# Optimization experiments

Measured on AMD Instinct MI355X. Metric: run time of the kernel, lower is better.

## Reference

```python
import jax, jax.numpy as jnp
import numpy as np
import math

D_MODEL = 1024
N_HEADS = 16
D_K = D_MODEL // N_HEADS
B, S = 4, 2048
NEG_INF = -1e9


def setup_inputs() -> dict:
    key = jax.random.key(0)
    ks = jax.random.split(key, 12)
    scale = 1.0 / math.sqrt(D_MODEL)
    inp = {
        "q": jax.random.normal(ks[0], (B, S, D_MODEL), jnp.float32),
        "k": jax.random.normal(ks[1], (B, S, D_MODEL), jnp.float32),
        "v": jax.random.normal(ks[2], (B, S, D_MODEL), jnp.float32),
        "mask": jax.random.randint(ks[3], (1, 1, S, S), 0, 2, jnp.int32),
        "w_q": jax.random.normal(ks[4], (D_MODEL, D_MODEL), jnp.float32) * scale,
        "b_q": jnp.zeros((D_MODEL,), jnp.float32),
        "w_k": jax.random.normal(ks[5], (D_MODEL, D_MODEL), jnp.float32) * scale,
        "b_k": jnp.zeros((D_MODEL,), jnp.float32),
        "w_v": jax.random.normal(ks[6], (D_MODEL, D_MODEL), jnp.float32) * scale,
        "b_v": jnp.zeros((D_MODEL,), jnp.float32),
        "w_o": jax.random.normal(ks[7], (D_MODEL, D_MODEL), jnp.float32) * scale,
        "b_o": jnp.zeros((D_MODEL,), jnp.float32),
    }
    return inp


def reference(q, k, v, mask, w_q, b_q, w_k, b_k, w_v, b_v, w_o, b_o):
    # Linear projections (torch Linear: x @ W.T + b)
    query = q @ w_q.T + b_q
    key_p = k @ w_k.T + b_k
    value = v @ w_v.T + b_v
    # [B,S,D] -> [B,H,S,d_k]
    def split_heads(x):
        return x.reshape(B, S, N_HEADS, D_K).transpose(0, 2, 1, 3)
    qh, kh, vh = split_heads(query), split_heads(key_p), split_heads(value)
    # scores: [B,H,S,S]
    scores = jnp.einsum('bhqd,bhkd->bhqk', qh, kh) / math.sqrt(D_K)
    scores = jnp.where(mask == 0, NEG_INF, scores)
    probs = jax.nn.softmax(scores, axis=-1)
    # attention output: [B,H,S,d_k] -> [B,S,D]
    x = jnp.einsum('bhqk,bhkd->bhqd', probs, vh)
    x = x.transpose(0, 2, 1, 3).reshape(B, S, D_MODEL)
    return x @ w_o.T + b_o
```

## Files before the change

kernel.cpp:

```cpp
#include <hip/hip_runtime.h>


typedef __bf16  bf16x8 __attribute__((ext_vector_type(8)));
typedef float   f32x4  __attribute__((ext_vector_type(4)));
typedef float   f32x16 __attribute__((ext_vector_type(16)));
typedef float   fv4    __attribute__((ext_vector_type(4)));
typedef unsigned int uint;
typedef __attribute__((address_space(3))) char        as3c;
typedef __attribute__((address_space(1))) const char  as1c;

static __device__ __forceinline__ void gload16(const void* g, void* l) {
  __builtin_amdgcn_global_load_lds((as1c*)g, (as3c*)l, 16, 0, 0);
}
static __device__ __forceinline__ f32x4 mfma16(bf16x8 a, bf16x8 b, f32x4 c) {
  return __builtin_amdgcn_mfma_f32_16x16x32_bf16(a, b, c, 0, 0, 0);
}
static __device__ __forceinline__ f32x16 mfma32(bf16x8 a, bf16x8 b, f32x16 c) {
  return __builtin_amdgcn_mfma_f32_32x32x16_bf16(a, b, c, 0, 0, 0);
}
static __device__ __forceinline__ void st4bf(void* dst, float a, float b, float c, float d) {
  union { __bf16 h[4]; unsigned long long u; } x;
  x.h[0] = (__bf16)a; x.h[1] = (__bf16)b; x.h[2] = (__bf16)c; x.h[3] = (__bf16)d;
  *(unsigned long long*)dst = x.u;
}
static __device__ __forceinline__ uint pk2(float lo, float hi) {
  union { __bf16 h[2]; uint u; } x;
  x.h[0] = (__bf16)lo; x.h[1] = (__bf16)hi; return x.u;
}
static __device__ __forceinline__ f32x16 fzero16() {
  f32x16 z;
#pragma unroll
  for (int i = 0; i < 16; ++i) z[i] = 0.f;
  return z;
}

__global__ void cvt_w(const float* __restrict__ w0, const float* __restrict__ w1,
                      const float* __restrict__ w2, const float* __restrict__ w3,
                      __bf16* __restrict__ dst) {
  int i = (blockIdx.x * 256 + threadIdx.x) * 4;
  int seg = i >> 20, off = i & 1048575;
  const float* s = seg == 0 ? w0 : seg == 1 ? w1 : seg == 2 ? w2 : w3;
  fv4 v = *(const fv4*)(s + off);
  st4bf(dst + i, v[0], v[1], v[2], v[3]);
}

__global__ void pack_mask(const int* __restrict__ mask,
                          unsigned long long* __restrict__ out) {
  int wid = threadIdx.x >> 6, lane = threadIdx.x & 63;
  for (int w = blockIdx.x * 4 + wid; w < 2048 * 32; w += gridDim.x * 4) {
    int v = mask[(w >> 5) * 2048 + (w & 31) * 64 + lane];
    unsigned long long bits = __ballot(v != 0);
    if (lane == 0) out[w] = bits;
  }
}

template<int MODE>
__global__ __launch_bounds__(256, 2)
void gemm_bt(const void* __restrict__ Ap, const __bf16* __restrict__ Bw,
             const float* __restrict__ bias, void* __restrict__ Cp) {
  __shared__ __align__(16) char lds_a[8192];
  __shared__ __align__(16) char lds_b[8192];
  const int t = threadIdx.x;
  const int lane = t & 63, lr = lane & 15, lg = lane >> 4;
  const int wid = t >> 6, wr = wid >> 1, wc = wid & 1;
  const int rowStart = blockIdx.x * 128, colStart = blockIdx.y * 128;

  f32x4 acc[4][4];
#pragma unroll
  for (int m = 0; m < 4; ++m)
#pragma unroll
    for (int n = 0; n < 4; ++n) {
      acc[m][n][0] = 0.f; acc[m][n][1] = 0.f; acc[m][n][2] = 0.f; acc[m][n][3] = 0.f;
    }

  for (int kt = 0; kt < 1024; kt += 32) {
    __syncthreads();
    if constexpr (MODE < 3) {
      const float* A = (const float*)Ap;
#pragma unroll
      for (int rr = 0; rr < 4; ++rr) {
        int lin = rr * 1024 + t * 4;
        int row = lin >> 5, col = lin & 31;
        fv4 v = *(const fv4*)(A + (rowStart + row) * 1024 + kt + col);
        st4bf(lds_a + lin * 2, v[0], v[1], v[2], v[3]);
      }
    } else {
      const __bf16* A = (const __bf16*)Ap;
#pragma unroll
      for (int rr = 0; rr < 2; ++rr) {
        int lin = rr * 2048 + t * 8;
        int row = lin >> 5, col = lin & 31;
        gload16(A + (rowStart + row) * 1024 + kt + col, lds_a + lin * 2);
      }
    }
#pragma unroll
    for (int rr = 0; rr < 2; ++rr) {
      int lin = rr * 2048 + t * 8;
      int row = lin >> 5, col = lin & 31;
      gload16(Bw + (colStart + row) * 1024 + kt + col, lds_b + lin * 2);
    }
    __syncthreads();

    bf16x8 af[4], bfr[4];
#pragma unroll
    for (int m = 0; m < 4; ++m)
      af[m] = *(const bf16x8*)(lds_a + (wr * 64 + m * 16 + lr) * 64 + lg * 16);
#pragma unroll
    for (int n = 0; n < 4; ++n)
      bfr[n] = *(const bf16x8*)(lds_b + (wc * 64 + n * 16 + lr) * 64 + lg * 16);
#pragma unroll
    for (int m = 0; m < 4; ++m)
#pragma unroll
      for (int n = 0; n < 4; ++n)
        acc[m][n] = mfma16(af[m], bfr[n], acc[m][n]);
  }

#pragma unroll
  for (int n = 0; n < 4; ++n) {
    int col = colStart + wc * 64 + n * 16 + lr;
    float bv = bias[col];
#pragma unroll
    for (int m = 0; m < 4; ++m) {
      int rowb = rowStart + wr * 64 + m * 16 + lg * 4;
      if constexpr (MODE == 0 || MODE == 1) {
        __bf16* C = (__bf16*)Cp;
#pragma unroll
        for (int r = 0; r < 4; ++r) {
          float val = acc[m][n][r] + bv;
          if constexpr (MODE == 0) val *= 0.125f;
          C[(rowb + r) * 1024 + col] = (__bf16)val;
        }
      } else if constexpr (MODE == 2) {
        __bf16* C = (__bf16*)Cp;
        int bb = rowb >> 11, s = rowb & 2047;
        st4bf(C + ((bb << 10) + col) * 2048 + s,
              acc[m][n][0] + bv, acc[m][n][1] + bv,
              acc[m][n][2] + bv, acc[m][n][3] + bv);
      } else {
        float* C = (float*)Cp;
#pragma unroll
        for (int r = 0; r < 4; ++r)
          C[(rowb + r) * 1024 + col] = acc[m][n][r] + bv;
      }
    }
  }
}

__global__ __launch_bounds__(256, 4)
void attn_fwd(const __bf16* __restrict__ Qp, const __bf16* __restrict__ Kp,
              const __bf16* __restrict__ Vt, const unsigned long long* __restrict__ Mb,
              __bf16* __restrict__ Xb) {
  __shared__ __align__(16) char lds[2][16384];
  const int t = threadIdx.x;
  const int lane = t & 63;
  const int l31 = lane & 31, hi = lane >> 5;
  const int wid = t >> 6;
  const int qblk = blockIdx.x, bh = blockIdx.y;
  const int b = bh >> 4, h = bh & 15;
  const int q = qblk * 128 + wid * 32 + l31;

  bf16x8 qf[4];
#pragma unroll
  for (int c = 0; c < 4; ++c)
    qf[c] = *(const bf16x8*)(Qp + (b * 2048 + q) * 1024 + h * 64 + c * 16 + hi * 8);

  f32x16 xacc0 = fzero16(), xacc1 = fzero16();
  float m_r = -__builtin_inff(), l_r = 0.f;

  auto stage = [&](int buf, int k0) {
#pragma unroll
    for (int rr = 0; rr < 2; ++rr) {
      int o = rr * 4096 + t * 16;
      int row = o >> 7, cb = o & 127;
      int cbs = cb ^ ((row & 7) << 4);
      gload16(Kp + (b * 2048 + k0 + row) * 1024 + h * 64 + (cbs >> 1), &lds[buf][o]);
      gload16(Vt + (bh * 64 + row) * 2048 + k0 + (cbs >> 1), &lds[buf][8192 + o]);
    }
  };

  stage(0, 0);
  int cur = 0;
  for (int it = 0; it < 32; ++it) {
    __syncthreads();
    if (it + 1 < 32) stage(cur ^ 1, (it + 1) * 64);

    const char* lk = lds[cur];
    const char* lv = lds[cur] + 8192;

    f32x16 sc0 = fzero16(), sc1 = fzero16();
#pragma unroll
    for (int c = 0; c < 4; ++c) {
      {
        int krow = l31;
        int byo = (c * 32 + hi * 16) ^ ((krow & 7) << 4);
        bf16x8 kf = *(const bf16x8*)(lk + krow * 128 + byo);
        sc0 = mfma32(kf, qf[c], sc0);
      }
      {
        int krow = 32 + l31;
        int byo = (c * 32 + hi * 16) ^ ((krow & 7) << 4);
        bf16x8 kf = *(const bf16x8*)(lk + krow * 128 + byo);
        sc1 = mfma32(kf, qf[c], sc1);
      }
    }

    unsigned long long mw = Mb[q * 32 + it];
    uint mm0 = ((uint)mw) >> (4 * hi);
    uint mm1 = ((uint)(mw >> 32)) >> (4 * hi);
    float rm = -1e30f;
#pragma unroll
    for (int r = 0; r < 16; ++r) {
      const int bit = (r & 3) + 8 * (r >> 2);
      float s0 = ((mm0 >> bit) & 1u) ? sc0[r] : -1e9f;
      float s1 = ((mm1 >> bit) & 1u) ? sc1[r] : -1e9f;
      sc0[r] = s0; sc1[r] = s1;
      rm = fmaxf(rm, fmaxf(s0, s1));
    }
    rm = fmaxf(rm, __shfl_xor(rm, 32));
    float mn = fmaxf(m_r, rm);
    float corr = __expf(m_r - mn);
    m_r = mn;
    float rs = 0.f;
#pragma unroll
    for (int r = 0; r < 16; ++r) {
      float p0 = __expf(sc0[r] - mn);
      float p1 = __expf(sc1[r] - mn);
      sc0[r] = p0; sc1[r] = p1;
      rs += p0 + p1;
    }
    rs += __shfl_xor(rs, 32);
    l_r = l_r * corr + rs;
    xacc0 = xacc0 * corr;
    xacc1 = xacc1 * corr;

    uint cp0[8], cp1[8];
#pragma unroll
    for (int m = 0; m < 8; ++m) {
      cp0[m] = pk2(sc0[2 * m], sc0[2 * m + 1]);
      cp1[m] = pk2(sc1[2 * m], sc1[2 * m + 1]);
    }

#define PV_SLICE(CPK, S) do {                                               \
      uint w0 = CPK[4 * ((S) & 1) + 0], w2 = CPK[4 * ((S) & 1) + 2];        \
      uint w1 = CPK[4 * ((S) & 1) + 1], w3 = CPK[4 * ((S) & 1) + 3];        \
      asm volatile("v_permlane32_swap_b32 %0, %1" : "+v"(w0), "+v"(w2));    \
      asm volatile("v_permlane32_swap_b32 %0, %1" : "+v"(w1), "+v"(w3));    \
      union { uint u[4]; bf16x8 v8; } pu;                                   \
      pu.u[0] = w0; pu.u[1] = w1; pu.u[2] = w2; pu.u[3] = w3;               \
      { int vrow = l31;                                                     \
        int byo = ((S) * 32 + hi * 16) ^ ((vrow & 7) << 4);                 \
        bf16x8 vf = *(const bf16x8*)(lv + vrow * 128 + byo);                \
        xacc0 = mfma32(vf, pu.v8, xacc0); }                                 \
      { int vrow = 32 + l31;                                                \
        int byo = ((S) * 32 + hi * 16) ^ ((vrow & 7) << 4);                 \
        bf16x8 vf = *(const bf16x8*)(lv + vrow * 128 + byo);                \
        xacc1 = mfma32(vf, pu.v8, xacc1); }                                 \
    } while (0)
    PV_SLICE(cp0, 0); PV_SLICE(cp0, 1); PV_SLICE(cp1, 2); PV_SLICE(cp1, 3);
#undef PV_SLICE
    cur ^= 1;
  }

  float inv = 1.f / l_r;
  __bf16* orow = Xb + (b * 2048 + q) * 1024 + h * 64 + 4 * hi;
#pragma unroll
  for (int g = 0; g < 4; ++g) {
    st4bf(orow + 8 * g,      xacc0[4 * g] * inv, xacc0[4 * g + 1] * inv,
                             xacc0[4 * g + 2] * inv, xacc0[4 * g + 3] * inv);
    st4bf(orow + 32 + 8 * g, xacc1[4 * g] * inv, xacc1[4 * g + 1] * inv,
                             xacc1[4 * g + 2] * inv, xacc1[4 * g + 3] * inv);
  }
}

extern "C" void kernel_launch(void* const* d_in, const int* in_sizes, int n_in,
                              void* d_out, int out_size, void* d_ws, size_t ws_size,
                              hipStream_t stream) {
  const float* q    = (const float*)d_in[0];
  const float* k    = (const float*)d_in[1];
  const float* v    = (const float*)d_in[2];
  const int*   mask = (const int*)d_in[3];
  const float* wq   = (const float*)d_in[4];
  const float* bq   = (const float*)d_in[5];
  const float* wk   = (const float*)d_in[6];
  const float* bk   = (const float*)d_in[7];
  const float* wv   = (const float*)d_in[8];
  const float* bv   = (const float*)d_in[9];
  const float* wo   = (const float*)d_in[10];
  const float* bo   = (const float*)d_in[11];

  char* ws = (char*)d_ws;
  __bf16* Wb  = (__bf16*)(ws);
  __bf16* Qp  = (__bf16*)(ws + (size_t)(8u  << 20));
  __bf16* Kp  = (__bf16*)(ws + (size_t)(24u << 20));
  __bf16* Vtb = (__bf16*)(ws + (size_t)(40u << 20));
  __bf16* Xb  = (__bf16*)(ws + (size_t)(56u << 20));
  unsigned long long* Mb = (unsigned long long*)(ws + (size_t)(72u << 20));

  cvt_w<<<4096, 256, 0, stream>>>(wq, wk, wv, wo, Wb);
  pack_mask<<<1024, 256, 0, stream>>>(mask, Mb);
  gemm_bt<0><<<dim3(64, 8), 256, 0, stream>>>(q, Wb,                 bq, Qp);
  gemm_bt<1><<<dim3(64, 8), 256, 0, stream>>>(k, Wb + (1u << 20),    bk, Kp);
  gemm_bt<2><<<dim3(64, 8), 256, 0, stream>>>(v, Wb + (2u << 20),    bv, Vtb);
  attn_fwd<<<dim3(16, 64), 256, 0, stream>>>(Qp, Kp, Vtb, Mb, Xb);
  gemm_bt<3><<<dim3(64, 8), 256, 0, stream>>>(Xb, Wb + (3u << 20),   bo, (float*)d_out);
}
```

Measured before the change: 445.5 us.

## Double-buffer GEMM loads, remap block order, and add lazy-rescale exp2 softmax

The GEMM now double-buffers its LDS tiles and prefetches the next K tile (A through registers, B through global_load_lds) while the current one is computed, to hide global load latency. GEMM and attention grids are flattened and remapped with an XCD-aware swizzle to improve L2 locality. The attention softmax folds log2(e) into the Q scale, uses exp2, rescales the accumulators only when the running max grows by more than a threshold, and applies the mask by bitwise-zeroing the probabilities. Occupancy hint drops from 4 to 3 blocks. The lazy rescale relies on fp32 headroom, and rows that are fully masked would now give zero sums instead of a uniform softmax.

Result: no change. 443.4 us (-0.5%).

```diff
diff --git a/kernel.cpp b/kernel.cpp
--- a/kernel.cpp
+++ b/kernel.cpp
@@ -58,61 +58,86 @@
 __global__ __launch_bounds__(256, 2)
 void gemm_bt(const void* __restrict__ Ap, const __bf16* __restrict__ Bw,
              const float* __restrict__ bias, void* __restrict__ Cp) {
-  __shared__ __align__(16) char lds_a[8192];
-  __shared__ __align__(16) char lds_b[8192];
+  __shared__ __align__(16) char lds_a[2][8192];
+  __shared__ __align__(16) char lds_b[2][8192];
   const int t = threadIdx.x;
   const int lane = t & 63, lr = lane & 15, lg = lane >> 4;
   const int wid = t >> 6, wr = wid >> 1, wc = wid & 1;
-  const int rowStart = blockIdx.x * 128, colStart = blockIdx.y * 128;
-
-  f32x4 acc[4][4];
-#pragma unroll
-  for (int m = 0; m < 4; ++m)
-#pragma unroll
-    for (int n = 0; n < 4; ++n) {
-      acc[m][n][0] = 0.f; acc[m][n][1] = 0.f; acc[m][n][2] = 0.f; acc[m][n][3] = 0.f;
-    }
-
-  for (int kt = 0; kt < 1024; kt += 32) {
-    __syncthreads();
+  const int bid = blockIdx.x;
+  const int nid = (bid & 7) * 64 + (bid >> 3);
+  const int rowStart = (nid & 63) * 128, colStart = (nid >> 6) * 128;
+
+  const float*  Af = (const float*)Ap;
+  const __bf16* Ah = (const __bf16*)Ap;
+  fv4 ra[4];
+
+  auto loadA = [&](int kt) {
     if constexpr (MODE < 3) {
-      const float* A = (const float*)Ap;
 #pragma unroll
       for (int rr = 0; rr < 4; ++rr) {
         int lin = rr * 1024 + t * 4;
         int row = lin >> 5, col = lin & 31;
-        fv4 v = *(const fv4*)(A + (rowStart + row) * 1024 + kt + col);
-        st4bf(lds_a + lin * 2, v[0], v[1], v[2], v[3]);
-      }
-    } else {
-      const __bf16* A = (const __bf16*)Ap;
+        ra[rr] = *(const fv4*)(Af + (rowStart + row) * 1024 + kt + col);
+      }
+    }
+  };
+  auto writeA = [&](int buf) {
+    if constexpr (MODE < 3) {
+#pragma unroll
+      for (int rr = 0; rr < 4; ++rr) {
+        int lin = rr * 1024 + t * 4;
+        st4bf(&lds_a[buf][lin * 2], ra[rr][0], ra[rr][1], ra[rr][2], ra[rr][3]);
+      }
+    }
+  };
+  auto stageAB = [&](int buf, int kt) {
+    if constexpr (MODE == 3) {
 #pragma unroll
       for (int rr = 0; rr < 2; ++rr) {
         int lin = rr * 2048 + t * 8;
         int row = lin >> 5, col = lin & 31;
-        gload16(A + (rowStart + row) * 1024 + kt + col, lds_a + lin * 2);
+        gload16(Ah + (rowStart + row) * 1024 + kt + col, &lds_a[buf][lin * 2]);
       }
     }
 #pragma unroll
     for (int rr = 0; rr < 2; ++rr) {
       int lin = rr * 2048 + t * 8;
       int row = lin >> 5, col = lin & 31;
-      gload16(Bw + (colStart + row) * 1024 + kt + col, lds_b + lin * 2);
-    }
+      gload16(Bw + (colStart + row) * 1024 + kt + col, &lds_b[buf][lin * 2]);
+    }
+  };
+
+  f32x4 acc[4][4];
+#pragma unroll
+  for (int m = 0; m < 4; ++m)
+#pragma unroll
+    for (int n = 0; n < 4; ++n) {
+      acc[m][n][0] = 0.f; acc[m][n][1] = 0.f; acc[m][n][2] = 0.f; acc[m][n][3] = 0.f;
+    }
+
+  loadA(0); stageAB(0, 0);
+  int cur = 0;
+  for (int it = 0; it < 32; ++it) {
     __syncthreads();
+    if constexpr (MODE < 3) {
+      writeA(cur);
+      __syncthreads();
+    }
+    if (it + 1 < 32) { loadA((it + 1) * 32); stageAB(cur ^ 1, (it + 1) * 32); }
 
     bf16x8 af[4], bfr[4];
 #pragma unroll
     for (int m = 0; m < 4; ++m)
-      af[m] = *(const bf16x8*)(lds_a + (wr * 64 + m * 16 + lr) * 64 + lg * 16);
+      af[m] = *(const bf16x8*)(&lds_a[cur][(wr * 64 + m * 16 + lr) * 64 + lg * 16]);
 #pragma unroll
     for (int n = 0; n < 4; ++n)
-      bfr[n] = *(const bf16x8*)(lds_b + (wc * 64 + n * 16 + lr) * 64 + lg * 16);
+      bfr[n] = *(const bf16x8*)(&lds_b[cur][(wc * 64 + n * 16 + lr) * 64 + lg * 16]);
 #pragma unroll
     for (int m = 0; m < 4; ++m)
 #pragma unroll
       for (int n = 0; n < 4; ++n)
         acc[m][n] = mfma16(af[m], bfr[n], acc[m][n]);
+    cur ^= 1;
   }
 
 #pragma unroll
@@ -127,7 +152,7 @@
 #pragma unroll
         for (int r = 0; r < 4; ++r) {
           float val = acc[m][n][r] + bv;
-          if constexpr (MODE == 0) val *= 0.125f;
+          if constexpr (MODE == 0) val *= 0.18033688011112042f;
           C[(rowb + r) * 1024 + col] = (__bf16)val;
         }
       } else if constexpr (MODE == 2) {
@@ -146,7 +171,7 @@
   }
 }
 
-__global__ __launch_bounds__(256, 4)
+__global__ __launch_bounds__(256, 3)
 void attn_fwd(const __bf16* __restrict__ Qp, const __bf16* __restrict__ Kp,
               const __bf16* __restrict__ Vt, const unsigned long long* __restrict__ Mb,
               __bf16* __restrict__ Xb) {
@@ -155,7 +180,9 @@
   const int lane = t & 63;
   const int l31 = lane & 31, hi = lane >> 5;
   const int wid = t >> 6;
-  const int qblk = blockIdx.x, bh = blockIdx.y;
+  const int bid = blockIdx.x;
+  const int nid = (bid & 7) * 128 + (bid >> 3);
+  const int qblk = nid & 15, bh = nid >> 4;
   const int b = bh >> 4, h = bh & 15;
   const int q = qblk * 128 + wid * 32 + l31;
 
@@ -165,7 +192,7 @@
     qf[c] = *(const bf16x8*)(Qp + (b * 2048 + q) * 1024 + h * 64 + c * 16 + hi * 8);
 
   f32x16 xacc0 = fzero16(), xacc1 = fzero16();
-  float m_r = -__builtin_inff(), l_r = 0.f;
+  float m_r = -1e30f, l_r = 0.f;
 
   auto stage = [&](int buf, int k0) {
 #pragma unroll
@@ -204,34 +231,38 @@
       }
     }
 
+    float rm = -1e30f;
+#pragma unroll
+    for (int r = 0; r < 16; ++r) rm = fmaxf(rm, fmaxf(sc0[r], sc1[r]));
+    rm = fmaxf(rm, __shfl_xor(rm, 32));
+
+    if (__any(rm > m_r + 8.f)) {
+      float mn = fmaxf(m_r, rm);
+      float corr = __builtin_amdgcn_exp2f(m_r - mn);
+      m_r = mn;
+      l_r *= corr;
+      xacc0 = xacc0 * corr;
+      xacc1 = xacc1 * corr;
+    }
+
     unsigned long long mw = Mb[q * 32 + it];
     uint mm0 = ((uint)mw) >> (4 * hi);
     uint mm1 = ((uint)(mw >> 32)) >> (4 * hi);
-    float rm = -1e30f;
+    float rs = 0.f;
 #pragma unroll
     for (int r = 0; r < 16; ++r) {
       const int bit = (r & 3) + 8 * (r >> 2);
-      float s0 = ((mm0 >> bit) & 1u) ? sc0[r] : -1e9f;
-      float s1 = ((mm1 >> bit) & 1u) ? sc1[r] : -1e9f;
-      sc0[r] = s0; sc1[r] = s1;
-      rm = fmaxf(rm, fmaxf(s0, s1));
-    }
-    rm = fmaxf(rm, __shfl_xor(rm, 32));
-    float mn = fmaxf(m_r, rm);
-    float corr = __expf(m_r - mn);
-    m_r = mn;
-    float rs = 0.f;
-#pragma unroll
-    for (int r = 0; r < 16; ++r) {
-      float p0 = __expf(sc0[r] - mn);
-      float p1 = __expf(sc1[r] - mn);
+      float p0 = __builtin_amdgcn_exp2f(sc0[r] - m_r);
+      float p1 = __builtin_amdgcn_exp2f(sc1[r] - m_r);
+      uint z0 = (uint)((int)(mm0 << (31 - bit)) >> 31);
+      uint z1 = (uint)((int)(mm1 << (31 - bit)) >> 31);
+      p0 = __uint_as_float(__float_as_uint(p0) & z0);
+      p1 = __uint_as_float(__float_as_uint(p1) & z1);
       sc0[r] = p0; sc1[r] = p1;
       rs += p0 + p1;
     }
     rs += __shfl_xor(rs, 32);
-    l_r = l_r * corr + rs;
-    xacc0 = xacc0 * corr;
-    xacc1 = xacc1 * corr;
+    l_r += rs;
 
     uint cp0[8], cp1[8];
 #pragma unroll
@@ -248,11 +279,11 @@
       union { uint u[4]; bf16x8 v8; } pu;                                   \
       pu.u[0] = w0; pu.u[1] = w1; pu.u[2] = w2; pu.u[3] = w3;               \
       { int vrow = l31;                                                     \
-        int byo = ((S) * 32 + hi * 16) ^ ((vrow & 7) << 4);                 \
+        int byo = (((S) * 32 + hi * 16)) ^ ((vrow & 7) << 4);               \
         bf16x8 vf = *(const bf16x8*)(lv + vrow * 128 + byo);                \
         xacc0 = mfma32(vf, pu.v8, xacc0); }                                 \
       { int vrow = 32 + l31;                                                \
-        int byo = ((S) * 32 + hi * 16) ^ ((vrow & 7) << 4);                 \
+        int byo = (((S) * 32 + hi * 16)) ^ ((vrow & 7) << 4);               \
         bf16x8 vf = *(const bf16x8*)(lv + vrow * 128 + byo);                \
         xacc1 = mfma32(vf, pu.v8, xacc1); }                                 \
     } while (0)
@@ -298,9 +329,9 @@
 
   cvt_w<<<4096, 256, 0, stream>>>(wq, wk, wv, wo, Wb);
   pack_mask<<<1024, 256, 0, stream>>>(mask, Mb);
-  gemm_bt<0><<<dim3(64, 8), 256, 0, stream>>>(q, Wb,                 bq, Qp);
-  gemm_bt<1><<<dim3(64, 8), 256, 0, stream>>>(k, Wb + (1u << 20),    bk, Kp);
-  gemm_bt<2><<<dim3(64, 8), 256, 0, stream>>>(v, Wb + (2u << 20),    bv, Vtb);
-  attn_fwd<<<dim3(16, 64), 256, 0, stream>>>(Qp, Kp, Vtb, Mb, Xb);
-  gemm_bt<3><<<dim3(64, 8), 256, 0, stream>>>(Xb, Wb + (3u << 20),   bo, (float*)d_out);
-}
+  gemm_bt<0><<<512, 256, 0, stream>>>(q, Wb,              bq, Qp);
+  gemm_bt<1><<<512, 256, 0, stream>>>(k, Wb + (1u << 20), bk, Kp);
+  gemm_bt<2><<<512, 256, 0, stream>>>(v, Wb + (2u << 20), bv, Vtb);
+  attn_fwd<<<1024, 256, 0, stream>>>(Qp, Kp, Vtb, Mb, Xb);
+  gemm_bt<3><<<512, 256, 0, stream>>>(Xb, Wb + (3u << 20), bo, (float*)d_out);
+}
```
